# Performance work log

Hardware: AMD Instinct MI355X
Metric: run time of the kernel (lower is better)

## Reference

```python
import jax, jax.numpy as jnp
import numpy as np

N_NODES = 32768
N_EDGES = 524288
HID = 128


def _linear_params(key, fan_in, fan_out):
    kw, kb = jax.random.split(key)
    bound = 1.0 / np.sqrt(fan_in)
    w = jax.random.uniform(kw, (fan_in, fan_out), jnp.float32, -bound, bound)
    b = jax.random.uniform(kb, (fan_out,), jnp.float32, -bound, bound)
    return w, b


def setup_inputs() -> dict:
    key = jax.random.key(0)
    ks = jax.random.split(key, 8)
    x = jax.random.normal(ks[0], (N_NODES, HID), jnp.float32)
    edge_attr = jax.random.normal(ks[1], (N_EDGES, HID), jnp.float32)
    edges = jax.random.randint(ks[2], (2, N_EDGES), 0, N_NODES, jnp.int32)
    w1, b1 = _linear_params(ks[3], 3 * HID, HID)      # message_fn layer 1
    w2, b2 = _linear_params(ks[4], HID, HID)          # message_fn layer 2
    wu1, bu1 = _linear_params(ks[5], HID, 2 * HID)    # update_fn layer 1
    wu2, bu2 = _linear_params(ks[6], 2 * HID, HID)    # update_fn layer 2
    return {"x": x, "edge_attr": edge_attr, "edges": edges,
            "w1": w1, "b1": b1, "w2": w2, "b2": b2,
            "wu1": wu1, "bu1": bu1, "wu2": wu2, "bu2": bu2}


def reference(x, edge_attr, edges, w1, b1, w2, b2, wu1, bu1, wu2, bu2):
    n_nodes = x.shape[0]
    send, recv = edges[0], edges[1]
    # gather endpoint features and concat with edge attributes: [E, 3*HID]
    ea = jnp.concatenate([x[send], x[recv], edge_attr], axis=-1)
    # per-edge message MLP (Linear-SiLU-Linear-SiLU)
    h = jax.nn.silu(ea @ w1 + b1)
    msg = jax.nn.silu(h @ w2 + b2)                    # [E, HID]
    # scatter-mean into receiving nodes
    sums = jax.ops.segment_sum(msg, recv, num_segments=n_nodes)
    counts = jax.ops.segment_sum(jnp.ones((msg.shape[0],), msg.dtype), recv,
                                 num_segments=n_nodes)
    aggr = sums / jnp.maximum(counts, 1.0)[:, None]
    # residual (input_size == hidden_size -> Identity) + update MLP
    xo = x + aggr
    xo = xo + (jax.nn.silu(xo @ wu1 + bu1) @ wu2 + bu2)
    return xo, msg
```

## Files before the change

kernel.cpp:

```cpp
#include <hip/hip_runtime.h>
#include <hip/hip_bf16.h>

#define NN 32768
#define NE 524288
#define HID 128

typedef unsigned short u16;
typedef unsigned int u32;
typedef __bf16 bf16x8 __attribute__((ext_vector_type(8)));
typedef float f32x4 __attribute__((ext_vector_type(4)));

__device__ __forceinline__ u16 f2bf(float f) {
  return __builtin_bit_cast(u16, (__bf16)f);
}
__device__ __forceinline__ float bf2f(u16 h) {
  return __builtin_bit_cast(float, (u32)h << 16);
}
__device__ __forceinline__ float silu_f(float v) {
  return v * __builtin_amdgcn_rcpf(1.f + __expf(-v));
}
__device__ __forceinline__ bf16x8 cvt8(float4 a, float4 b) {
  bf16x8 r;
  r[0] = (__bf16)a.x; r[1] = (__bf16)a.y; r[2] = (__bf16)a.z; r[3] = (__bf16)a.w;
  r[4] = (__bf16)b.x; r[5] = (__bf16)b.y; r[6] = (__bf16)b.z; r[7] = (__bf16)b.w;
  return r;
}
__device__ __forceinline__ float4 f4fma(float4 x, float4 s, float inv) {
  return make_float4(x.x + s.x * inv, x.y + s.y * inv,
                     x.z + s.z * inv, x.w + s.w * inv);
}

__device__ __forceinline__ void gld16(const void* g, void* l) {
  __builtin_amdgcn_global_load_lds(
      (const __attribute__((address_space(1))) u32*)g,
      (__attribute__((address_space(3))) u32*)l, 16, 0, 0);
}

#define WL()   do { asm volatile("s_waitcnt lgkmcnt(0)" ::: "memory"); \
                    __builtin_amdgcn_sched_barrier(0); } while (0)

__global__ __launch_bounds__(256) void prep_k(
    const float* __restrict__ x, const float* __restrict__ w1,
    const float* __restrict__ w2, const float* __restrict__ wu1,
    const float* __restrict__ wu2, const int* __restrict__ recv,
    u16* __restrict__ xb, u16* __restrict__ w1Ts, u16* __restrict__ w2Ts,
    u16* __restrict__ wu1T, u16* __restrict__ wu2T, int* __restrict__ cnt)
{
  int i = blockIdx.x * 256 + threadIdx.x;
  xb[i] = f2bf(x[i]);
  if (i < NE) atomicAdd(&cnt[recv[i]], 1);
  if (i < 3 * 128 * 128) {
    int j = i & 7, qs = (i >> 3) & 15, c = (i >> 7) & 127, s = i >> 14;
    int k = s * 128 + ((qs ^ (c & 7)) << 3) + j;
    w1Ts[i] = f2bf(w1[k * 128 + c]);
  }
  if (i < 128 * 128) {
    int j = i & 7, qs = (i >> 3) & 15, c = i >> 7;
    int k = ((qs ^ (c & 7)) << 3) + j;
    w2Ts[i] = f2bf(w2[k * 128 + c]);
  }
  if (i < 256 * 128) { int c = i >> 7, k = i & 127; wu1T[i] = f2bf(wu1[k * 256 + c]); }
  if (i < 128 * 256) { int c = i >> 8, k = i & 255; wu2T[i] = f2bf(wu2[k * 128 + c]); }
}

__global__ __launch_bounds__(1024) void scan_k(const int* __restrict__ cnt,
                                               int* __restrict__ cursor)
{
  __shared__ int part[1024];
  const int tid = threadIdx.x;
  const int base = tid * 32;
  int v[32];
  int s = 0;
  #pragma unroll
  for (int j = 0; j < 32; ++j) { v[j] = cnt[base + j]; s += v[j]; }
  part[tid] = s;
  __syncthreads();
  #pragma unroll 1
  for (int d = 1; d < 1024; d <<= 1) {
    int t = (tid >= d) ? part[tid - d] : 0;
    __syncthreads();
    part[tid] += t;
    __syncthreads();
  }
  int ex = part[tid] - s;
  #pragma unroll
  for (int j = 0; j < 32; ++j) {
    cursor[base + j] = ex;
    ex += v[j];
  }
}

__global__ __launch_bounds__(256) void scatter_k(const int* __restrict__ send,
                                                 const int* __restrict__ recv,
                                                 int* __restrict__ cursor,
                                                 int* __restrict__ eperm,
                                                 int* __restrict__ sid,
                                                 int* __restrict__ rid)
{
  int e = blockIdx.x * 256 + threadIdx.x;
  int r = recv[e];
  int s = send[e];
  int pos = atomicAdd(&cursor[r], 1);
  eperm[pos] = e;
  sid[pos] = s;
  rid[pos] = r;
}

__global__ __launch_bounds__(512, 2) void edge_mlp(
    const u16* __restrict__ xb, const float* __restrict__ eattr,
    const int* __restrict__ eperm, const int* __restrict__ sid,
    const int* __restrict__ rid,
    const u16* __restrict__ wTs, const float* __restrict__ b1,
    const float* __restrict__ b2,
    float* __restrict__ msg_out, float* __restrict__ sums)
{
  __shared__ u16 sW[65536];
  __shared__ u16 sT[8][1280];

  const int tid  = threadIdx.x;
  const int lane = tid & 63;
  const int w    = tid >> 6;
  const int fr   = lane & 15;
  const int fkq  = lane >> 4;
  const int orow = fkq * 4;
  const int half = lane >> 5;
  const int cloc = lane & 31;

  #pragma unroll
  for (int i = 0; i < 16; ++i)
    gld16(wTs + (size_t)(i * 512 + tid) * 8, sW + (size_t)(i * 512 + w * 64) * 8);
  asm volatile("s_waitcnt vmcnt(0)" ::: "memory");
  __builtin_amdgcn_s_barrier();

  float b1v[8], b2v[8];
  #pragma unroll
  for (int n = 0; n < 8; ++n) {
    b1v[n] = b1[n * 16 + fr];
    b2v[n] = b2[n * 16 + fr];
  }

  const int xcd = blockIdx.x & 7, jj = blockIdx.x >> 3;
  int base = (xcd * 2048 + (jj * 8 + w) * 8) * 32;

  int eoA = eperm[base + fr], eoB = eperm[base + 16 + fr];
  int nsA = sid[base + fr],   nsB = sid[base + 16 + fr];
  int nrA = rid[base + fr],   nrB = rid[base + 16 + fr];

  bf16x8 a0[4][2], a1[4][2];
  #pragma unroll
  for (int kk = 0; kk < 4; ++kk) {
    a0[kk][0] = *reinterpret_cast<const bf16x8*>(xb + (size_t)nsA * 128 + kk * 32 + fkq * 8);
    a0[kk][1] = *reinterpret_cast<const bf16x8*>(xb + (size_t)nsB * 128 + kk * 32 + fkq * 8);
    a1[kk][0] = *reinterpret_cast<const bf16x8*>(xb + (size_t)nrA * 128 + kk * 32 + fkq * 8);
    a1[kk][1] = *reinterpret_cast<const bf16x8*>(xb + (size_t)nrB * 128 + kk * 32 + fkq * 8);
  }

  u16* tch = &sT[w][0];

  auto slice = [&](const bf16x8 (&A)[4][2], int P, f32x4 (&C)[2][8]) {
    #pragma unroll
    for (int kk = 0; kk < 4; ++kk) {
      bf16x8 bF[8];
      #pragma unroll
      for (int n = 0; n < 8; ++n) {
        int c = n * 16 + fr;
        int ch = (kk * 4 + fkq) ^ (c & 7);
        bF[n] = __builtin_bit_cast(bf16x8,
            *reinterpret_cast<const uint4*>(sW + P * 16384 + (c << 7) + (ch << 3)));
      }
      __builtin_amdgcn_s_setprio(1);
      #pragma unroll
      for (int m = 0; m < 2; ++m)
        #pragma unroll
        for (int n = 0; n < 8; ++n)
          C[m][n] = __builtin_amdgcn_mfma_f32_16x16x32_bf16(A[kk][m], bF[n], C[m][n], 0, 0, 0);
      __builtin_amdgcn_s_setprio(0);
    }
  };

  #pragma unroll 1
  for (int t = 0; t < 8; ++t) {
    float4 ea[2][8];
    const float* epA = eattr + ((size_t)eoA << 7) + fkq * 8;
    const float* epB = eattr + ((size_t)eoB << 7) + fkq * 8;
    #pragma unroll
    for (int kk = 0; kk < 4; ++kk) {
      ea[0][2 * kk]     = *reinterpret_cast<const float4*>(epA + kk * 32);
      ea[0][2 * kk + 1] = *reinterpret_cast<const float4*>(epA + kk * 32 + 4);
      ea[1][2 * kk]     = *reinterpret_cast<const float4*>(epB + kk * 32);
      ea[1][2 * kk + 1] = *reinterpret_cast<const float4*>(epB + kk * 32 + 4);
    }
    int eg[2][4];
    #pragma unroll
    for (int m = 0; m < 2; ++m)
      #pragma unroll
      for (int r = 0; r < 4; ++r)
        eg[m][r] = eperm[base + m * 16 + orow + r];
    int nid[16];
    #pragma unroll
    for (int r = 0; r < 16; ++r) nid[r] = rid[base + half * 16 + r];
    int base1 = (t < 7) ? base + 32 : base;
    int eoA1 = eperm[base1 + fr], eoB1 = eperm[base1 + 16 + fr];
    int nsA1 = sid[base1 + fr],   nsB1 = sid[base1 + 16 + fr];
    int nrA1 = rid[base1 + fr],   nrB1 = rid[base1 + 16 + fr];
    __builtin_amdgcn_sched_barrier(0);

    f32x4 acc[2][8];
    #pragma unroll
    for (int m = 0; m < 2; ++m)
      #pragma unroll
      for (int n = 0; n < 8; ++n)
        #pragma unroll
        for (int r = 0; r < 4; ++r) acc[m][n][r] = 0.f;

    slice(a0, 0, acc);
    slice(a1, 1, acc);
    bf16x8 ae[4][2];
    #pragma unroll
    for (int kk = 0; kk < 4; ++kk) {
      ae[kk][0] = cvt8(ea[0][2 * kk], ea[0][2 * kk + 1]);
      ae[kk][1] = cvt8(ea[1][2 * kk], ea[1][2 * kk + 1]);
    }
    slice(ae, 2, acc);

    f32x4 acc2[2][8];
    #pragma unroll
    for (int m = 0; m < 2; ++m)
      #pragma unroll
      for (int n = 0; n < 8; ++n)
        #pragma unroll
        for (int r = 0; r < 4; ++r) acc2[m][n][r] = 0.f;

    #pragma unroll
    for (int kk = 0; kk < 4; ++kk) {
      #pragma unroll
      for (int m = 0; m < 2; ++m)
        #pragma unroll
        for (int nl = 0; nl < 2; ++nl) {
          int n = 2 * kk + nl;
          #pragma unroll
          for (int r = 0; r < 4; ++r)
            tch[(m * 16 + orow + r) * 40 + nl * 16 + fr] =
                f2bf(silu_f(acc[m][n][r] + b1v[n]));
        }
      WL();
      bf16x8 ah[2];
      ah[0] = __builtin_bit_cast(bf16x8,
          *reinterpret_cast<const uint4*>(tch + fr * 40 + fkq * 8));
      ah[1] = __builtin_bit_cast(bf16x8,
          *reinterpret_cast<const uint4*>(tch + (16 + fr) * 40 + fkq * 8));
      bf16x8 bF[8];
      #pragma unroll
      for (int n = 0; n < 8; ++n) {
        int c = n * 16 + fr;
        int ch = (kk * 4 + fkq) ^ (c & 7);
        bF[n] = __builtin_bit_cast(bf16x8,
            *reinterpret_cast<const uint4*>(sW + 3 * 16384 + (c << 7) + (ch << 3)));
      }
      __builtin_amdgcn_s_setprio(1);
      #pragma unroll
      for (int m = 0; m < 2; ++m)
        #pragma unroll
        for (int n = 0; n < 8; ++n)
          acc2[m][n] = __builtin_amdgcn_mfma_f32_16x16x32_bf16(ah[m], bF[n], acc2[m][n], 0, 0, 0);
      __builtin_amdgcn_s_setprio(0);
    }

    #pragma unroll
    for (int kk = 0; kk < 4; ++kk) {
      a0[kk][0] = *reinterpret_cast<const bf16x8*>(xb + (size_t)nsA1 * 128 + kk * 32 + fkq * 8);
      a0[kk][1] = *reinterpret_cast<const bf16x8*>(xb + (size_t)nsB1 * 128 + kk * 32 + fkq * 8);
      a1[kk][0] = *reinterpret_cast<const bf16x8*>(xb + (size_t)nrA1 * 128 + kk * 32 + fkq * 8);
      a1[kk][1] = *reinterpret_cast<const bf16x8*>(xb + (size_t)nrB1 * 128 + kk * 32 + fkq * 8);
    }
    __builtin_amdgcn_sched_barrier(0);

    #pragma unroll
    for (int cc = 0; cc < 4; ++cc) {
      #pragma unroll
      for (int m = 0; m < 2; ++m)
        #pragma unroll
        for (int nl = 0; nl < 2; ++nl) {
          int n = 2 * cc + nl;
          #pragma unroll
          for (int r = 0; r < 4; ++r) {
            float v = silu_f(acc2[m][n][r] + b2v[n]);
            msg_out[((size_t)eg[m][r] << 7) + n * 16 + fr] = v;
            tch[(m * 16 + orow + r) * 40 + nl * 16 + fr] = f2bf(v);
          }
        }
      WL();
      float s = 0.f;
      int cur = nid[0];
      #pragma unroll
      for (int r = 0; r < 16; ++r) {
        s += bf2f(tch[(half * 16 + r) * 40 + cloc]);
        int nxt = (r < 15) ? nid[r + 1] : -1;
        if (nxt != cur) {
          atomicAdd(sums + (size_t)cur * HID + cc * 32 + cloc, s);
          s = 0.f;
          cur = nxt;
        }
      }
      WL();
    }

    base = base1;
    eoA = eoA1; eoB = eoB1;
  }
}

__global__ __launch_bounds__(256) void mlp1_k(
    const float* __restrict__ x, const float* __restrict__ sums,
    const int* __restrict__ cnt, const u16* __restrict__ wu1T,
    const float* __restrict__ bu1, u16* __restrict__ t)
{
  __shared__ u16 sB[256][40];
  const int tid = threadIdx.x, lane = tid & 63, wid = tid >> 6;
  const int wr = wid >> 1, wc = wid & 1;
  const int fr = lane & 15, fkq = lane >> 4, fk = fkq * 8, orow = fkq * 4;
  const int n0 = blockIdx.x * 64;

  float invm[2];
  #pragma unroll
  for (int m = 0; m < 2; ++m)
    invm[m] = __builtin_amdgcn_rcpf(fmaxf((float)cnt[n0 + wr * 32 + m * 16 + fr], 1.f));

  f32x4 acc[2][8];
  #pragma unroll
  for (int m = 0; m < 2; ++m)
    #pragma unroll
    for (int n = 0; n < 8; ++n)
      #pragma unroll
      for (int r = 0; r < 4; ++r) acc[m][n][r] = 0.f;

  #pragma unroll 1
  for (int kk = 0; kk < 4; ++kk) {
    #pragma unroll
    for (int it = 0; it < 4; ++it) {
      int chunk = tid + it * 256;
      int c = chunk >> 2, q = chunk & 3;
      *reinterpret_cast<uint4*>(&sB[c][q * 8]) =
          *reinterpret_cast<const uint4*>(wu1T + c * 128 + kk * 32 + q * 8);
    }
    __syncthreads();
    bf16x8 aF[2], bF[8];
    #pragma unroll
    for (int m = 0; m < 2; ++m) {
      size_t basei = (size_t)(n0 + wr * 32 + m * 16 + fr) * HID + kk * 32 + fk;
      float4 xv0 = *reinterpret_cast<const float4*>(x + basei);
      float4 xv1 = *reinterpret_cast<const float4*>(x + basei + 4);
      float4 sv0 = *reinterpret_cast<const float4*>(sums + basei);
      float4 sv1 = *reinterpret_cast<const float4*>(sums + basei + 4);
      aF[m] = cvt8(f4fma(xv0, sv0, invm[m]), f4fma(xv1, sv1, invm[m]));
    }
    #pragma unroll
    for (int n = 0; n < 8; ++n)
      bF[n] = __builtin_bit_cast(bf16x8,
          *reinterpret_cast<const uint4*>(&sB[wc * 128 + n * 16 + fr][fk]));
    #pragma unroll
    for (int m = 0; m < 2; ++m)
      #pragma unroll
      for (int n = 0; n < 8; ++n)
        acc[m][n] = __builtin_amdgcn_mfma_f32_16x16x32_bf16(aF[m], bF[n], acc[m][n], 0, 0, 0);
    __syncthreads();
  }
  #pragma unroll
  for (int n = 0; n < 8; ++n) {
    int col = wc * 128 + n * 16 + fr;
    float bb = bu1[col];
    #pragma unroll
    for (int m = 0; m < 2; ++m) {
      int row = n0 + wr * 32 + m * 16 + orow;
      #pragma unroll
      for (int r = 0; r < 4; ++r)
        t[(size_t)(row + r) * 256 + col] = f2bf(silu_f(acc[m][n][r] + bb));
    }
  }
}

__global__ __launch_bounds__(256) void mlp2_k(
    const u16* __restrict__ t, const u16* __restrict__ wu2T,
    const float* __restrict__ bu2, const float* __restrict__ x,
    const float* __restrict__ sums, const int* __restrict__ cnt,
    float* __restrict__ xo)
{
  __shared__ u16 sB[128][40];
  const int tid = threadIdx.x, lane = tid & 63, wid = tid >> 6;
  const int wr = wid >> 1, wc = wid & 1;
  const int fr = lane & 15, fk = (lane >> 4) * 8, orow = (lane >> 4) * 4;
  const int n0 = blockIdx.x * 64;

  f32x4 acc[2][4];
  #pragma unroll
  for (int m = 0; m < 2; ++m)
    #pragma unroll
    for (int n = 0; n < 4; ++n)
      #pragma unroll
      for (int r = 0; r < 4; ++r) acc[m][n][r] = 0.f;

  #pragma unroll 1
  for (int kk = 0; kk < 8; ++kk) {
    #pragma unroll
    for (int it = 0; it < 2; ++it) {
      int chunk = tid + it * 256;
      int c = chunk >> 2, q = chunk & 3;
      *reinterpret_cast<uint4*>(&sB[c][q * 8]) =
          *reinterpret_cast<const uint4*>(wu2T + c * 256 + kk * 32 + q * 8);
    }
    __syncthreads();
    bf16x8 aF[2], bF[4];
    #pragma unroll
    for (int m = 0; m < 2; ++m)
      aF[m] = __builtin_bit_cast(bf16x8, *reinterpret_cast<const uint4*>(
          t + (size_t)(n0 + wr * 32 + m * 16 + fr) * 256 + kk * 32 + fk));
    #pragma unroll
    for (int n = 0; n < 4; ++n)
      bF[n] = __builtin_bit_cast(bf16x8,
          *reinterpret_cast<const uint4*>(&sB[wc * 64 + n * 16 + fr][fk]));
    #pragma unroll
    for (int m = 0; m < 2; ++m)
      #pragma unroll
      for (int n = 0; n < 4; ++n)
        acc[m][n] = __builtin_amdgcn_mfma_f32_16x16x32_bf16(aF[m], bF[n], acc[m][n], 0, 0, 0);
    __syncthreads();
  }
  #pragma unroll
  for (int m = 0; m < 2; ++m) {
    #pragma unroll
    for (int r = 0; r < 4; ++r) {
      int gn = n0 + wr * 32 + m * 16 + orow + r;
      float inv = 1.f / fmaxf((float)cnt[gn], 1.f);
      #pragma unroll
      for (int n = 0; n < 4; ++n) {
        int col = wc * 64 + n * 16 + fr;
        float xi = x[(size_t)gn * HID + col] + sums[(size_t)gn * HID + col] * inv;
        xo[(size_t)gn * HID + col] = xi + acc[m][n][r] + bu2[col];
      }
    }
  }
}

extern "C" void kernel_launch(void* const* d_in, const int* in_sizes, int n_in,
                              void* d_out, int out_size, void* d_ws, size_t ws_size,
                              hipStream_t stream)
{
  (void)in_sizes; (void)n_in; (void)out_size; (void)ws_size;
  const float* x     = (const float*)d_in[0];
  const float* eattr = (const float*)d_in[1];
  const int*   edges = (const int*)d_in[2];
  const float* w1  = (const float*)d_in[3];
  const float* b1  = (const float*)d_in[4];
  const float* w2  = (const float*)d_in[5];
  const float* b2  = (const float*)d_in[6];
  const float* wu1 = (const float*)d_in[7];
  const float* bu1 = (const float*)d_in[8];
  const float* wu2 = (const float*)d_in[9];
  const float* bu2 = (const float*)d_in[10];

  float* xo  = (float*)d_out;
  float* msg = xo + (size_t)NN * HID;

  char* p = (char*)d_ws;
  u16* xb    = (u16*)p; p += (size_t)NN * HID * 2;
  u16* w1Ts  = (u16*)p; p += 384 * 128 * 2;
  u16* w2Ts  = (u16*)p; p += 128 * 128 * 2;
  u16* wu1T  = (u16*)p; p += 256 * 128 * 2;
  u16* wu2T  = (u16*)p; p += 128 * 256 * 2;
  u16* tbuf  = (u16*)p; p += (size_t)NN * 256 * 2;
  float* sums = (float*)p; p += (size_t)NN * HID * 4;
  int* cnt    = (int*)p; p += (size_t)NN * 4;
  int* cursor = (int*)p; p += (size_t)NN * 4;
  int* eperm  = (int*)p; p += (size_t)NE * 4;
  int* sid    = (int*)p; p += (size_t)NE * 4;
  int* rid    = (int*)p; p += (size_t)NE * 4;

  const int* send = edges;
  const int* recv = edges + NE;

  hipMemsetAsync(cnt, 0, (size_t)NN * 4, stream);
  hipMemsetAsync(sums, 0, (size_t)NN * HID * 4, stream);
  prep_k<<<NN * HID / 256, 256, 0, stream>>>(x, w1, w2, wu1, wu2, recv,
                                             xb, w1Ts, w2Ts, wu1T, wu2T, cnt);
  scan_k<<<1, 1024, 0, stream>>>(cnt, cursor);
  scatter_k<<<NE / 256, 256, 0, stream>>>(send, recv, cursor, eperm, sid, rid);
  edge_mlp<<<256, 512, 0, stream>>>(xb, eattr, eperm, sid, rid,
                                    w1Ts, b1, b2, msg, sums);
  mlp1_k<<<NN / 64, 256, 0, stream>>>(x, sums, cnt, wu1T, bu1, tbuf);
  mlp2_k<<<NN / 64, 256, 0, stream>>>(tbuf, wu2T, bu2, x, sums, cnt, xo);
}
```

Measured before the change: 297.1 us.

## Double edge_mlp block to 1024 threads, swizzle tile LDS, coalesce msg stores

Grows the edge MLP block from 8 to 16 waves so each block processes its tiles with twice the waves and half the loop trips. The per-wave LDS tile shrinks from padded 40-column rows to 32-column rows with an XOR swizzle. The message output is now written as coalesced float4 rows read back from the bf16 LDS tile, replacing scattered per-element fp32 stores. In exchange the stored msg passes through bf16 rounding, which loses precision. The launch bound of 1024 threads caps registers per thread and may cause spills.

```diff
diff --git a/kernel.cpp b/kernel.cpp
--- a/kernel.cpp
+++ b/kernel.cpp
@@ -106,7 +106,7 @@
   rid[pos] = r;
 }
 
-__global__ __launch_bounds__(512, 2) void edge_mlp(
+__global__ __launch_bounds__(1024, 4) void edge_mlp(
     const u16* __restrict__ xb, const float* __restrict__ eattr,
     const int* __restrict__ eperm, const int* __restrict__ sid,
     const int* __restrict__ rid,
@@ -115,7 +115,7 @@
     float* __restrict__ msg_out, float* __restrict__ sums)
 {
   __shared__ u16 sW[65536];
-  __shared__ u16 sT[8][1280];
+  __shared__ u16 sT[16][1024];
 
   const int tid  = threadIdx.x;
   const int lane = tid & 63;
@@ -125,10 +125,14 @@
   const int orow = fkq * 4;
   const int half = lane >> 5;
   const int cloc = lane & 31;
-
-  #pragma unroll
-  for (int i = 0; i < 16; ++i)
-    gld16(wTs + (size_t)(i * 512 + tid) * 8, sW + (size_t)(i * 512 + w * 64) * 8);
+  const int row2 = lane >> 1;
+  const int cg   = (lane & 1) * 16;
+
+  #pragma unroll
+  for (int i = 0; i < 8; ++i) {
+    int c = i * 16 + w;
+    gld16(wTs + (size_t)c * 512 + lane * 8, sW + (size_t)c * 512);
+  }
   asm volatile("s_waitcnt vmcnt(0)" ::: "memory");
   __builtin_amdgcn_s_barrier();
 
@@ -140,7 +144,7 @@
   }
 
   const int xcd = blockIdx.x & 7, jj = blockIdx.x >> 3;
-  int base = (xcd * 2048 + (jj * 8 + w) * 8) * 32;
+  int base = xcd * 65536 + (jj * 16 + w) * 128;
 
   int eoA = eperm[base + fr], eoB = eperm[base + 16 + fr];
   int nsA = sid[base + fr],   nsB = sid[base + 16 + fr];
@@ -179,7 +183,7 @@
   };
 
   #pragma unroll 1
-  for (int t = 0; t < 8; ++t) {
+  for (int t = 0; t < 4; ++t) {
     float4 ea[2][8];
     const float* epA = eattr + ((size_t)eoA << 7) + fkq * 8;
     const float* epB = eattr + ((size_t)eoB << 7) + fkq * 8;
@@ -190,16 +194,11 @@
       ea[1][2 * kk]     = *reinterpret_cast<const float4*>(epB + kk * 32);
       ea[1][2 * kk + 1] = *reinterpret_cast<const float4*>(epB + kk * 32 + 4);
     }
-    int eg[2][4];
-    #pragma unroll
-    for (int m = 0; m < 2; ++m)
-      #pragma unroll
-      for (int r = 0; r < 4; ++r)
-        eg[m][r] = eperm[base + m * 16 + orow + r];
+    int egv = eperm[base + row2];
     int nid[16];
     #pragma unroll
     for (int r = 0; r < 16; ++r) nid[r] = rid[base + half * 16 + r];
-    int base1 = (t < 7) ? base + 32 : base;
+    int base1 = (t < 3) ? base + 32 : base;
     int eoA1 = eperm[base1 + fr], eoB1 = eperm[base1 + 16 + fr];
     int nsA1 = sid[base1 + fr],   nsB1 = sid[base1 + 16 + fr];
     int nrA1 = rid[base1 + fr],   nrB1 = rid[base1 + 16 + fr];
@@ -238,17 +237,20 @@
         #pragma unroll
         for (int nl = 0; nl < 2; ++nl) {
           int n = 2 * kk + nl;
+          int c2 = nl * 2 + (fr >> 3);
           #pragma unroll
-          for (int r = 0; r < 4; ++r)
-            tch[(m * 16 + orow + r) * 40 + nl * 16 + fr] =
+          for (int r = 0; r < 4; ++r) {
+            int row = m * 16 + orow + r;
+            tch[row * 32 + ((c2 ^ (row & 3)) << 3) + (fr & 7)] =
                 f2bf(silu_f(acc[m][n][r] + b1v[n]));
+          }
         }
       WL();
       bf16x8 ah[2];
-      ah[0] = __builtin_bit_cast(bf16x8,
-          *reinterpret_cast<const uint4*>(tch + fr * 40 + fkq * 8));
-      ah[1] = __builtin_bit_cast(bf16x8,
-          *reinterpret_cast<const uint4*>(tch + (16 + fr) * 40 + fkq * 8));
+      ah[0] = __builtin_bit_cast(bf16x8, *reinterpret_cast<const uint4*>(
+          tch + fr * 32 + ((fkq ^ (fr & 3)) << 3)));
+      ah[1] = __builtin_bit_cast(bf16x8, *reinterpret_cast<const uint4*>(
+          tch + (16 + fr) * 32 + ((fkq ^ (fr & 3)) << 3)));
       bf16x8 bF[8];
       #pragma unroll
       for (int n = 0; n < 8; ++n) {
@@ -282,24 +284,40 @@
         #pragma unroll
         for (int nl = 0; nl < 2; ++nl) {
           int n = 2 * cc + nl;
+          int c2 = nl * 2 + (fr >> 3);
           #pragma unroll
           for (int r = 0; r < 4; ++r) {
-            float v = silu_f(acc2[m][n][r] + b2v[n]);
-            msg_out[((size_t)eg[m][r] << 7) + n * 16 + fr] = v;
-            tch[(m * 16 + orow + r) * 40 + nl * 16 + fr] = f2bf(v);
+            int row = m * 16 + orow + r;
+            tch[row * 32 + ((c2 ^ (row & 3)) << 3) + (fr & 7)] =
+                f2bf(silu_f(acc2[m][n][r] + b2v[n]));
           }
         }
       WL();
-      float s = 0.f;
-      int cur = nid[0];
-      #pragma unroll
-      for (int r = 0; r < 16; ++r) {
-        s += bf2f(tch[(half * 16 + r) * 40 + cloc]);
-        int nxt = (r < 15) ? nid[r + 1] : -1;
-        if (nxt != cur) {
-          atomicAdd(sums + (size_t)cur * HID + cc * 32 + cloc, s);
-          s = 0.f;
-          cur = nxt;
+      {
+        float s = 0.f;
+        int cur = nid[0];
+        #pragma unroll
+        for (int r = 0; r < 16; ++r) {
+          int row = half * 16 + r;
+          s += bf2f(tch[row * 32 + ((((cloc >> 3) ^ (row & 3))) << 3) + (cloc & 7)]);
+          int nxt = (r < 15) ? nid[r + 1] : -1;
+          if (nxt != cur) {
+            atomicAdd(sums + (size_t)cur * HID + cc * 32 + cloc, s);
+            s = 0.f;
+            cur = nxt;
+          }
+        }
+      }
+      {
+        const u16* sp = tch + row2 * 32;
+        float* mp = msg_out + ((size_t)egv << 7) + cc * 32 + cg;
+        #pragma unroll
+        for (int i = 0; i < 4; ++i) {
+          int c2 = ((cg + i * 4) >> 3) ^ (row2 & 3);
+          int off = (c2 << 3) + ((i * 4) & 7);
+          float4 o = make_float4(bf2f(sp[off]), bf2f(sp[off + 1]),
+                                 bf2f(sp[off + 2]), bf2f(sp[off + 3]));
+          *reinterpret_cast<float4*>(mp + i * 4) = o;
         }
       }
       WL();
@@ -484,8 +502,8 @@
                                              xb, w1Ts, w2Ts, wu1T, wu2T, cnt);
   scan_k<<<1, 1024, 0, stream>>>(cnt, cursor);
   scatter_k<<<NE / 256, 256, 0, stream>>>(send, recv, cursor, eperm, sid, rid);
-  edge_mlp<<<256, 512, 0, stream>>>(xb, eattr, eperm, sid, rid,
-                                    w1Ts, b1, b2, msg, sums);
+  edge_mlp<<<256, 1024, 0, stream>>>(xb, eattr, eperm, sid, rid,
+                                     w1Ts, b1, b2, msg, sums);
   mlp1_k<<<NN / 64, 256, 0, stream>>>(x, sums, cnt, wu1T, bu1, tbuf);
   mlp2_k<<<NN / 64, 256, 0, stream>>>(tbuf, wu2T, bu2, x, sums, cnt, xo);
 }
```

Result: slower. 602.3 us (+102.7%).
